# Kernel optimization log

Hardware: AMD Instinct MI355X
Metric: run time of the kernel (lower is better)

The kernel has to match this reference:

```python
import jax, jax.numpy as jnp
import numpy as np

N_NODES = 100000
N_EDGES = 1600000
IN_F, HID_F, N_CLS = 512, 128, 64


def spmm(row, col, val, x, n):
    # out[i] = sum_{e: row[e]==i} val[e] * x[col[e]]  (sparse adj @ x)
    msgs = val[:, None] * x[col]          # [E, F] gather + scale
    return jax.ops.segment_sum(msgs, row, num_segments=n)


def setup_inputs() -> dict:
    key = jax.random.key(0)
    k = jax.random.split(key, 8)
    x = jax.random.normal(k[0], (N_NODES, IN_F), dtype=jnp.float32)
    adj_row = jax.random.randint(k[1], (N_EDGES,), 0, N_NODES, dtype=jnp.int32)
    adj_col = jax.random.randint(k[2], (N_EDGES,), 0, N_NODES, dtype=jnp.int32)
    adj_val = jax.random.uniform(k[3], (N_EDGES,), dtype=jnp.float32)
    s1 = 1.0 / np.sqrt(IN_F)
    s2 = 1.0 / np.sqrt(HID_F)
    w1 = jax.random.uniform(k[4], (IN_F, HID_F), jnp.float32, -s1, s1)
    b1 = jax.random.uniform(k[5], (HID_F,), jnp.float32, -s1, s1)
    w2 = jax.random.uniform(k[6], (HID_F, N_CLS), jnp.float32, -s2, s2)
    b2 = jax.random.uniform(k[7], (N_CLS,), jnp.float32, -s2, s2)
    return {"x": x, "adj_row": adj_row, "adj_col": adj_col, "adj_val": adj_val,
            "w1": w1, "b1": b1, "w2": w2, "b2": b2}


def reference(x, adj_row, adj_col, adj_val, w1, b1, w2, b2):
    n = x.shape[0]
    # conv1: dense projection then sparse aggregation
    h = spmm(adj_row, adj_col, adj_val, x @ w1 + b1, n)
    h = jax.nn.relu(h)  # dropout is identity in eval mode
    # conv2
    out = spmm(adj_row, adj_col, adj_val, h @ w2 + b2, n)
    return out
```

## Files before the change

kernel.cpp:

```cpp
#include <hip/hip_runtime.h>
#include <hip/hip_bf16.h>


constexpr int N_NODES = 100000;
constexpr int IN_F    = 512;
constexpr int HID_F   = 128;
constexpr int N_CLS   = 64;
constexpr int N_EDGES = 1600000;

constexpr int SCAN_BLOCK    = 256;
constexpr int N_SCAN_BLOCKS = (N_NODES + SCAN_BLOCK - 1) / SCAN_BLOCK;
constexpr int N_WAVES_G     = N_NODES / 32;

typedef __attribute__((ext_vector_type(8))) short short8;
typedef __attribute__((ext_vector_type(4))) float f32x4;

static __device__ __forceinline__ unsigned short f2bf(float x) {
    unsigned int u = __float_as_uint(x);
    unsigned int r = (u + 0x7FFFu + ((u >> 16) & 1u)) >> 16;
    return (unsigned short)r;
}
static __device__ __forceinline__ float bf2f(unsigned short u) {
    return __uint_as_float(((unsigned int)u) << 16);
}

__global__ void w1t_kernel(const float* __restrict__ w1, unsigned short* __restrict__ w1t)
{
    int idx = blockIdx.x * 256 + threadIdx.x;
    int n = idx >> 9, k = idx & 511;
    w1t[idx] = f2bf(w1[k * HID_F + n]);
}

__global__ void w2t_kernel(const float* __restrict__ w2, unsigned short* __restrict__ w2t)
{
    int idx = blockIdx.x * 256 + threadIdx.x;
    int n = idx >> 7, k = idx & 127;
    w2t[idx] = f2bf(w2[k * N_CLS + n]);
}

__global__ void zero_int_kernel(int* __restrict__ p, int n)
{
    int i = blockIdx.x * blockDim.x + threadIdx.x;
    if (i < n) p[i] = 0;
}

__global__ void hist_kernel(const int* __restrict__ row, int* __restrict__ counts)
{
    int e = blockIdx.x * blockDim.x + threadIdx.x;
    if (e < N_EDGES) atomicAdd(&counts[row[e]], 1);
}

__global__ __launch_bounds__(SCAN_BLOCK) void scanA_kernel(
    const int* __restrict__ counts, int* __restrict__ local_ex,
    int* __restrict__ blockSums)
{
    __shared__ int s[SCAN_BLOCK];
    const int t = threadIdx.x;
    const int i = blockIdx.x * SCAN_BLOCK + t;
    int v = (i < N_NODES) ? counts[i] : 0;
    s[t] = v;
    __syncthreads();
    for (int off = 1; off < SCAN_BLOCK; off <<= 1) {
        int u = (t >= off) ? s[t - off] : 0;
        __syncthreads();
        s[t] += u;
        __syncthreads();
    }
    if (i < N_NODES) local_ex[i] = s[t] - v;
    if (t == SCAN_BLOCK - 1) blockSums[blockIdx.x] = s[t];
}

__global__ __launch_bounds__(512) void scanB_kernel(int* __restrict__ blockSums)
{
    __shared__ int s[512];
    const int t = threadIdx.x;
    int v = (t < N_SCAN_BLOCKS) ? blockSums[t] : 0;
    s[t] = v;
    __syncthreads();
    for (int off = 1; off < 512; off <<= 1) {
        int u = (t >= off) ? s[t - off] : 0;
        __syncthreads();
        s[t] += u;
        __syncthreads();
    }
    if (t < N_SCAN_BLOCKS) blockSums[t] = s[t] - v;
}

__global__ __launch_bounds__(SCAN_BLOCK) void scanC_kernel(
    const int* __restrict__ local_ex, const int* __restrict__ blockSums,
    int* __restrict__ row_ptr, int* __restrict__ cursor)
{
    const int i = blockIdx.x * SCAN_BLOCK + threadIdx.x;
    if (i < N_NODES) {
        int v = local_ex[i] + blockSums[blockIdx.x];
        row_ptr[i] = v;
        cursor[i]  = v;
    }
    if (i == 0) row_ptr[N_NODES] = N_EDGES;
}

__global__ void scatter_kernel(
    const int* __restrict__ row, const int* __restrict__ col,
    const float* __restrict__ val, int* __restrict__ cursor,
    int2* __restrict__ es)
{
    int e = blockIdx.x * blockDim.x + threadIdx.x;
    if (e < N_EDGES) {
        int pos = atomicAdd(&cursor[row[e]], 1);
        es[pos] = make_int2(col[e], __float_as_int(val[e]));
    }
}

__global__ __launch_bounds__(256) void gemm1_mfma_kernel(
    const float* __restrict__ x, const unsigned short* __restrict__ w1t,
    const float* __restrict__ b1, unsigned short* __restrict__ h0b)
{
    const int lane = threadIdx.x & 63;
    const int wid  = blockIdx.x * 4 + (threadIdx.x >> 6);
    if (wid >= N_WAVES_G) return;
    const int row0 = wid * 32;
    const int m = lane & 15;
    const int q = lane >> 4;

    f32x4 acc[2][8];
#pragma unroll
    for (int mi = 0; mi < 2; ++mi)
#pragma unroll
        for (int ni = 0; ni < 8; ++ni)
            acc[mi][ni] = (f32x4){0.f, 0.f, 0.f, 0.f};

    union U8 { short8 v; __hip_bfloat162 h[4]; };

    const float* a0p = x + (size_t)(row0 + m)      * IN_F + q * 8;
    const float* a1p = x + (size_t)(row0 + 16 + m) * IN_F + q * 8;
    const unsigned short* bp = w1t + (size_t)m * IN_F + q * 8;

    float4 c0l = ((const float4*)a0p)[0];
    float4 c0h = ((const float4*)a0p)[1];
    float4 c1l = ((const float4*)a1p)[0];
    float4 c1h = ((const float4*)a1p)[1];

    for (int kk = 0; kk < IN_F; kk += 32) {
        short8 bf[8];
#pragma unroll
        for (int ni = 0; ni < 8; ++ni)
            bf[ni] = *(const short8*)(bp + (size_t)ni * 16 * IN_F + kk);

        float4 n0l, n0h, n1l, n1h;
        if (kk + 32 < IN_F) {
            n0l = ((const float4*)(a0p + kk + 32))[0];
            n0h = ((const float4*)(a0p + kk + 32))[1];
            n1l = ((const float4*)(a1p + kk + 32))[0];
            n1h = ((const float4*)(a1p + kk + 32))[1];
        }

        U8 u0, u1;
        u0.h[0] = __float22bfloat162_rn(make_float2(c0l.x, c0l.y));
        u0.h[1] = __float22bfloat162_rn(make_float2(c0l.z, c0l.w));
        u0.h[2] = __float22bfloat162_rn(make_float2(c0h.x, c0h.y));
        u0.h[3] = __float22bfloat162_rn(make_float2(c0h.z, c0h.w));
        u1.h[0] = __float22bfloat162_rn(make_float2(c1l.x, c1l.y));
        u1.h[1] = __float22bfloat162_rn(make_float2(c1l.z, c1l.w));
        u1.h[2] = __float22bfloat162_rn(make_float2(c1h.x, c1h.y));
        u1.h[3] = __float22bfloat162_rn(make_float2(c1h.z, c1h.w));
        short8 a0 = u0.v, a1 = u1.v;

#pragma unroll
        for (int ni = 0; ni < 8; ++ni) {
            acc[0][ni] = __builtin_amdgcn_mfma_f32_16x16x32_bf16(a0, bf[ni], acc[0][ni], 0, 0, 0);
            acc[1][ni] = __builtin_amdgcn_mfma_f32_16x16x32_bf16(a1, bf[ni], acc[1][ni], 0, 0, 0);
        }

        c0l = n0l; c0h = n0h; c1l = n1l; c1h = n1h;
    }

    float bias[8];
#pragma unroll
    for (int ni = 0; ni < 8; ++ni) bias[ni] = b1[ni * 16 + m];

#pragma unroll
    for (int mi = 0; mi < 2; ++mi)
#pragma unroll
        for (int r = 0; r < 4; ++r) {
            int row = row0 + mi * 16 + q * 4 + r;
            unsigned short* dst = h0b + (size_t)row * HID_F;
#pragma unroll
            for (int ni = 0; ni < 8; ++ni)
                dst[ni * 16 + m] = f2bf(acc[mi][ni][r] + bias[ni]);
        }
}

__global__ __launch_bounds__(256) void gemm2_mfma_kernel(
    const unsigned short* __restrict__ h1r, const unsigned short* __restrict__ w2t,
    const float* __restrict__ b2, float* __restrict__ h2)
{
    const int lane = threadIdx.x & 63;
    const int wid  = blockIdx.x * 4 + (threadIdx.x >> 6);
    if (wid >= N_WAVES_G) return;
    const int row0 = wid * 32;
    const int m = lane & 15;
    const int q = lane >> 4;

    f32x4 acc[2][4];
#pragma unroll
    for (int mi = 0; mi < 2; ++mi)
#pragma unroll
        for (int ni = 0; ni < 4; ++ni)
            acc[mi][ni] = (f32x4){0.f, 0.f, 0.f, 0.f};

    const unsigned short* a0p = h1r + (size_t)(row0 + m)      * HID_F + q * 8;
    const unsigned short* a1p = h1r + (size_t)(row0 + 16 + m) * HID_F + q * 8;
    const unsigned short* bp  = w2t + (size_t)m * HID_F + q * 8;

#pragma unroll
    for (int t = 0; t < 4; ++t) {
        short8 a0 = *(const short8*)(a0p + t * 32);
        short8 a1 = *(const short8*)(a1p + t * 32);
#pragma unroll
        for (int ni = 0; ni < 4; ++ni) {
            short8 b = *(const short8*)(bp + (size_t)ni * 16 * HID_F + t * 32);
            acc[0][ni] = __builtin_amdgcn_mfma_f32_16x16x32_bf16(a0, b, acc[0][ni], 0, 0, 0);
            acc[1][ni] = __builtin_amdgcn_mfma_f32_16x16x32_bf16(a1, b, acc[1][ni], 0, 0, 0);
        }
    }

    float bias[4];
#pragma unroll
    for (int ni = 0; ni < 4; ++ni) bias[ni] = b2[ni * 16 + m];

#pragma unroll
    for (int mi = 0; mi < 2; ++mi)
#pragma unroll
        for (int r = 0; r < 4; ++r) {
            int row = row0 + mi * 16 + q * 4 + r;
            float* dst = h2 + (size_t)row * N_CLS;
#pragma unroll
            for (int ni = 0; ni < 4; ++ni)
                dst[ni * 16 + m] = acc[mi][ni][r] + bias[ni];
        }
}

__global__ __launch_bounds__(256) void spmm_g128_kernel(
    const int* __restrict__ rp, const int2* __restrict__ es,
    const unsigned short* __restrict__ src, unsigned short* __restrict__ dst)
{
    const int r = blockIdx.x * 4 + threadIdx.y;
    if (r >= N_NODES) return;
    const int lane = threadIdx.x;
    const int j0 = rp[r], j1 = rp[r + 1];

    float ax = 0.f, ay = 0.f;
    int j = j0;
    for (; j + 7 < j1; j += 8) {
        int2 e[8];
        ushort2 u[8];
#pragma unroll
        for (int t = 0; t < 8; ++t) e[t] = es[j + t];
#pragma unroll
        for (int t = 0; t < 8; ++t)
            u[t] = ((const ushort2*)(src + (size_t)e[t].x * HID_F))[lane];
#pragma unroll
        for (int t = 0; t < 8; ++t) {
            float v = __int_as_float(e[t].y);
            ax += v * bf2f(u[t].x);
            ay += v * bf2f(u[t].y);
        }
    }
    if (j + 3 < j1) {
        int2 e[4];
        ushort2 u[4];
#pragma unroll
        for (int t = 0; t < 4; ++t) e[t] = es[j + t];
#pragma unroll
        for (int t = 0; t < 4; ++t)
            u[t] = ((const ushort2*)(src + (size_t)e[t].x * HID_F))[lane];
#pragma unroll
        for (int t = 0; t < 4; ++t) {
            float v = __int_as_float(e[t].y);
            ax += v * bf2f(u[t].x);
            ay += v * bf2f(u[t].y);
        }
        j += 4;
    }
    for (; j < j1; ++j) {
        int2 e = es[j];
        float v = __int_as_float(e.y);
        ushort2 u = ((const ushort2*)(src + (size_t)e.x * HID_F))[lane];
        ax += v * bf2f(u.x);
        ay += v * bf2f(u.y);
    }
    ushort2 o;
    o.x = f2bf(fmaxf(ax, 0.f));
    o.y = f2bf(fmaxf(ay, 0.f));
    ((ushort2*)(dst + (size_t)r * HID_F))[lane] = o;
}

__global__ __launch_bounds__(256) void spmm_g64_kernel(
    const int* __restrict__ rp, const int2* __restrict__ es,
    const float* __restrict__ src, float* __restrict__ dst)
{
    const int r = blockIdx.x * 4 + threadIdx.y;
    if (r >= N_NODES) return;
    const int lane = threadIdx.x;
    const int j0 = rp[r], j1 = rp[r + 1];

    float acc = 0.f;
    int j = j0;
    for (; j + 7 < j1; j += 8) {
        int2 e[8];
        float a[8];
#pragma unroll
        for (int t = 0; t < 8; ++t) e[t] = es[j + t];
#pragma unroll
        for (int t = 0; t < 8; ++t)
            a[t] = src[(size_t)e[t].x * N_CLS + lane];
#pragma unroll
        for (int t = 0; t < 8; ++t)
            acc += __int_as_float(e[t].y) * a[t];
    }
    if (j + 3 < j1) {
        int2 e[4];
        float a[4];
#pragma unroll
        for (int t = 0; t < 4; ++t) e[t] = es[j + t];
#pragma unroll
        for (int t = 0; t < 4; ++t)
            a[t] = src[(size_t)e[t].x * N_CLS + lane];
#pragma unroll
        for (int t = 0; t < 4; ++t)
            acc += __int_as_float(e[t].y) * a[t];
        j += 4;
    }
    for (; j < j1; ++j) {
        int2 e = es[j];
        acc += __int_as_float(e.y) * src[(size_t)e.x * N_CLS + lane];
    }
    dst[(size_t)r * N_CLS + lane] = acc;
}

extern "C" void kernel_launch(void* const* d_in, const int* in_sizes, int n_in,
                              void* d_out, int out_size, void* d_ws, size_t ws_size,
                              hipStream_t stream)
{
    const float* x       = (const float*)d_in[0];
    const int*   adj_row = (const int*)  d_in[1];
    const int*   adj_col = (const int*)  d_in[2];
    const float* adj_val = (const float*)d_in[3];
    const float* w1      = (const float*)d_in[4];
    const float* b1      = (const float*)d_in[5];
    const float* w2      = (const float*)d_in[6];
    const float* b2      = (const float*)d_in[7];
    float*       out     = (float*)d_out;

    char* ws = (char*)d_ws;
    unsigned short* h0b   = (unsigned short*)ws;
    unsigned short* h1r   = (unsigned short*)(ws + 25600000);
    float*          h2    = (float*)(ws + 51200000);
    int2*           es    = (int2*) (ws + 76800000);
    int*            rp    = (int*)  (ws + 89600000);
    int*            cur   = (int*)  (ws + 90000016);
    unsigned short* w1t   = (unsigned short*)(ws + 90400016);
    int*            lex   = (int*)  (ws + 90531088);
    int*            bsum  = (int*)  (ws + 90931088);
    unsigned short* w2t   = (unsigned short*)(ws + 90932656);

    w1t_kernel<<<IN_F * HID_F / 256, 256, 0, stream>>>(w1, w1t);
    w2t_kernel<<<HID_F * N_CLS / 256, 256, 0, stream>>>(w2, w2t);
    zero_int_kernel<<<(N_NODES + 255) / 256, 256, 0, stream>>>(cur, N_NODES);
    hist_kernel<<<(N_EDGES + 255) / 256, 256, 0, stream>>>(adj_row, cur);
    scanA_kernel<<<N_SCAN_BLOCKS, SCAN_BLOCK, 0, stream>>>(cur, lex, bsum);
    scanB_kernel<<<1, 512, 0, stream>>>(bsum);
    scanC_kernel<<<N_SCAN_BLOCKS, SCAN_BLOCK, 0, stream>>>(lex, bsum, rp, cur);
    scatter_kernel<<<(N_EDGES + 255) / 256, 256, 0, stream>>>(
        adj_row, adj_col, adj_val, cur, es);

    gemm1_mfma_kernel<<<(N_WAVES_G + 3) / 4, 256, 0, stream>>>(x, w1t, b1, h0b);
    spmm_g128_kernel<<<(N_NODES + 3) / 4, dim3(64, 4), 0, stream>>>(
        rp, es, h0b, h1r);

    gemm2_mfma_kernel<<<(N_WAVES_G + 3) / 4, 256, 0, stream>>>(h1r, w2t, b2, h2);
    spmm_g64_kernel<<<(N_NODES + 3) / 4, dim3(64, 4), 0, stream>>>(
        rp, es, h2, out);
}
```

Before: 688.3 us.

## Stage GEMM weight tiles in swizzled LDS shared across 8-wave blocks

Result: faster. 660.1 us (-4.1%).

```diff
diff --git a/kernel.cpp b/kernel.cpp
--- a/kernel.cpp
+++ b/kernel.cpp
@@ -10,7 +10,7 @@
 
 constexpr int SCAN_BLOCK    = 256;
 constexpr int N_SCAN_BLOCKS = (N_NODES + SCAN_BLOCK - 1) / SCAN_BLOCK;
-constexpr int N_WAVES_G     = N_NODES / 32;
+constexpr int NB_GEMM       = (N_NODES + 255) / 256;
 
 typedef __attribute__((ext_vector_type(8))) short short8;
 typedef __attribute__((ext_vector_type(4))) float f32x4;
@@ -111,16 +111,20 @@
     }
 }
 
-__global__ __launch_bounds__(256) void gemm1_mfma_kernel(
+__global__ __launch_bounds__(512, 4) void gemm1_mfma_kernel(
     const float* __restrict__ x, const unsigned short* __restrict__ w1t,
     const float* __restrict__ b1, unsigned short* __restrict__ h0b)
 {
-    const int lane = threadIdx.x & 63;
-    const int wid  = blockIdx.x * 4 + (threadIdx.x >> 6);
-    if (wid >= N_WAVES_G) return;
-    const int row0 = wid * 32;
+    __shared__ unsigned short Bs[128 * 256];
+    char* lb = (char*)Bs;
+
+    const int tid  = threadIdx.x;
+    const int lane = tid & 63;
+    const int w    = tid >> 6;
     const int m = lane & 15;
     const int q = lane >> 4;
+    const int row0 = blockIdx.x * 256 + w * 32;
+    const bool active = row0 < N_NODES;
 
     f32x4 acc[2][8];
 #pragma unroll
@@ -133,46 +137,67 @@
 
     const float* a0p = x + (size_t)(row0 + m)      * IN_F + q * 8;
     const float* a1p = x + (size_t)(row0 + 16 + m) * IN_F + q * 8;
-    const unsigned short* bp = w1t + (size_t)m * IN_F + q * 8;
-
-    float4 c0l = ((const float4*)a0p)[0];
-    float4 c0h = ((const float4*)a0p)[1];
-    float4 c1l = ((const float4*)a1p)[0];
-    float4 c1h = ((const float4*)a1p)[1];
-
-    for (int kk = 0; kk < IN_F; kk += 32) {
-        short8 bf[8];
-#pragma unroll
-        for (int ni = 0; ni < 8; ++ni)
-            bf[ni] = *(const short8*)(bp + (size_t)ni * 16 * IN_F + kk);
-
-        float4 n0l, n0h, n1l, n1h;
-        if (kk + 32 < IN_F) {
-            n0l = ((const float4*)(a0p + kk + 32))[0];
-            n0h = ((const float4*)(a0p + kk + 32))[1];
-            n1l = ((const float4*)(a1p + kk + 32))[0];
-            n1h = ((const float4*)(a1p + kk + 32))[1];
-        }
-
-        U8 u0, u1;
-        u0.h[0] = __float22bfloat162_rn(make_float2(c0l.x, c0l.y));
-        u0.h[1] = __float22bfloat162_rn(make_float2(c0l.z, c0l.w));
-        u0.h[2] = __float22bfloat162_rn(make_float2(c0h.x, c0h.y));
-        u0.h[3] = __float22bfloat162_rn(make_float2(c0h.z, c0h.w));
-        u1.h[0] = __float22bfloat162_rn(make_float2(c1l.x, c1l.y));
-        u1.h[1] = __float22bfloat162_rn(make_float2(c1l.z, c1l.w));
-        u1.h[2] = __float22bfloat162_rn(make_float2(c1h.x, c1h.y));
-        u1.h[3] = __float22bfloat162_rn(make_float2(c1h.z, c1h.w));
-        short8 a0 = u0.v, a1 = u1.v;
-
-#pragma unroll
-        for (int ni = 0; ni < 8; ++ni) {
-            acc[0][ni] = __builtin_amdgcn_mfma_f32_16x16x32_bf16(a0, bf[ni], acc[0][ni], 0, 0, 0);
-            acc[1][ni] = __builtin_amdgcn_mfma_f32_16x16x32_bf16(a1, bf[ni], acc[1][ni], 0, 0, 0);
-        }
-
-        c0l = n0l; c0h = n0h; c1l = n1l; c1h = n1h;
-    }
+    const int swz = (m & 7) << 4;
+
+    for (int p = 0; p < 2; ++p) {
+        {
+            const unsigned short* src = w1t + p * 256;
+#pragma unroll
+            for (int i = 0; i < 8; ++i) {
+                int chunk = tid + i * 512;
+                int n   = chunk >> 5;
+                int k16 = chunk & 31;
+                short8 v = *(const short8*)(src + (size_t)n * IN_F + k16 * 8);
+                *(short8*)(lb + ((n * 512 + k16 * 16) ^ ((n & 7) << 4))) = v;
+            }
+        }
+        __syncthreads();
+
+        if (active) {
+            const float* a0 = a0p + p * 256;
+            const float* a1 = a1p + p * 256;
+            float4 c0l = ((const float4*)a0)[0];
+            float4 c0h = ((const float4*)a0)[1];
+            float4 c1l = ((const float4*)a1)[0];
+            float4 c1h = ((const float4*)a1)[1];
+
+#pragma unroll
+            for (int t = 0; t < 8; ++t) {
+                float4 n0l, n0h, n1l, n1h;
+                if (t + 1 < 8) {
+                    n0l = ((const float4*)(a0 + (t + 1) * 32))[0];
+                    n0h = ((const float4*)(a0 + (t + 1) * 32))[1];
+                    n1l = ((const float4*)(a1 + (t + 1) * 32))[0];
+                    n1h = ((const float4*)(a1 + (t + 1) * 32))[1];
+                }
+
+                U8 u0, u1;
+                u0.h[0] = __float22bfloat162_rn(make_float2(c0l.x, c0l.y));
+                u0.h[1] = __float22bfloat162_rn(make_float2(c0l.z, c0l.w));
+                u0.h[2] = __float22bfloat162_rn(make_float2(c0h.x, c0h.y));
+                u0.h[3] = __float22bfloat162_rn(make_float2(c0h.z, c0h.w));
+                u1.h[0] = __float22bfloat162_rn(make_float2(c1l.x, c1l.y));
+                u1.h[1] = __float22bfloat162_rn(make_float2(c1l.z, c1l.w));
+                u1.h[2] = __float22bfloat162_rn(make_float2(c1h.x, c1h.y));
+                u1.h[3] = __float22bfloat162_rn(make_float2(c1h.z, c1h.w));
+                short8 av0 = u0.v, av1 = u1.v;
+
+                const int kb = t * 64 + q * 16;
+#pragma unroll
+                for (int ni = 0; ni < 8; ++ni) {
+                    int off = (((ni * 16 + m) * 512) + kb) ^ swz;
+                    short8 bfr = *(const short8*)(lb + off);
+                    acc[0][ni] = __builtin_amdgcn_mfma_f32_16x16x32_bf16(av0, bfr, acc[0][ni], 0, 0, 0);
+                    acc[1][ni] = __builtin_amdgcn_mfma_f32_16x16x32_bf16(av1, bfr, acc[1][ni], 0, 0, 0);
+                }
+
+                c0l = n0l; c0h = n0h; c1l = n1l; c1h = n1h;
+            }
+        }
+        __syncthreads();
+    }
+
+    if (!active) return;
 
     float bias[8];
 #pragma unroll
@@ -190,16 +215,41 @@
         }
 }
 
-__global__ __launch_bounds__(256) void gemm2_mfma_kernel(
+__global__ __launch_bounds__(512, 4) void gemm2_mfma_kernel(
     const unsigned short* __restrict__ h1r, const unsigned short* __restrict__ w2t,
     const float* __restrict__ b2, float* __restrict__ h2)
 {
-    const int lane = threadIdx.x & 63;
-    const int wid  = blockIdx.x * 4 + (threadIdx.x >> 6);
-    if (wid >= N_WAVES_G) return;
-    const int row0 = wid * 32;
+    __shared__ unsigned short Bs[64 * 128];
+    char* lb = (char*)Bs;
+
+    const int tid  = threadIdx.x;
+    const int lane = tid & 63;
+    const int w    = tid >> 6;
     const int m = lane & 15;
     const int q = lane >> 4;
+    const int row0 = blockIdx.x * 256 + w * 32;
+    const bool active = row0 < N_NODES;
+
+#pragma unroll
+    for (int i = 0; i < 2; ++i) {
+        int chunk = tid + i * 512;
+        int n   = chunk >> 4;
+        int k16 = chunk & 15;
+        short8 v = *(const short8*)(w2t + (size_t)n * HID_F + k16 * 8);
+        *(short8*)(lb + ((n * 256 + k16 * 16) ^ ((n & 7) << 4))) = v;
+    }
+    __syncthreads();
+    if (!active) return;
+
+    const unsigned short* a0p = h1r + (size_t)(row0 + m)      * HID_F + q * 8;
+    const unsigned short* a1p = h1r + (size_t)(row0 + 16 + m) * HID_F + q * 8;
+
+    short8 a0[4], a1[4];
+#pragma unroll
+    for (int t = 0; t < 4; ++t) {
+        a0[t] = *(const short8*)(a0p + t * 32);
+        a1[t] = *(const short8*)(a1p + t * 32);
+    }
 
     f32x4 acc[2][4];
 #pragma unroll
@@ -208,19 +258,16 @@
         for (int ni = 0; ni < 4; ++ni)
             acc[mi][ni] = (f32x4){0.f, 0.f, 0.f, 0.f};
 
-    const unsigned short* a0p = h1r + (size_t)(row0 + m)      * HID_F + q * 8;
-    const unsigned short* a1p = h1r + (size_t)(row0 + 16 + m) * HID_F + q * 8;
-    const unsigned short* bp  = w2t + (size_t)m * HID_F + q * 8;
-
+    const int swz = (m & 7) << 4;
 #pragma unroll
     for (int t = 0; t < 4; ++t) {
-        short8 a0 = *(const short8*)(a0p + t * 32);
-        short8 a1 = *(const short8*)(a1p + t * 32);
+        const int kb = t * 64 + q * 16;
 #pragma unroll
         for (int ni = 0; ni < 4; ++ni) {
-            short8 b = *(const short8*)(bp + (size_t)ni * 16 * HID_F + t * 32);
-            acc[0][ni] = __builtin_amdgcn_mfma_f32_16x16x32_bf16(a0, b, acc[0][ni], 0, 0, 0);
-            acc[1][ni] = __builtin_amdgcn_mfma_f32_16x16x32_bf16(a1, b, acc[1][ni], 0, 0, 0);
+            int off = (((ni * 16 + m) * 256) + kb) ^ swz;
+            short8 b = *(const short8*)(lb + off);
+            acc[0][ni] = __builtin_amdgcn_mfma_f32_16x16x32_bf16(a0[t], b, acc[0][ni], 0, 0, 0);
+            acc[1][ni] = __builtin_amdgcn_mfma_f32_16x16x32_bf16(a1[t], b, acc[1][ni], 0, 0, 0);
         }
     }
 
@@ -374,11 +421,11 @@
     scatter_kernel<<<(N_EDGES + 255) / 256, 256, 0, stream>>>(
         adj_row, adj_col, adj_val, cur, es);
 
-    gemm1_mfma_kernel<<<(N_WAVES_G + 3) / 4, 256, 0, stream>>>(x, w1t, b1, h0b);
+    gemm1_mfma_kernel<<<NB_GEMM, 512, 0, stream>>>(x, w1t, b1, h0b);
     spmm_g128_kernel<<<(N_NODES + 3) / 4, dim3(64, 4), 0, stream>>>(
         rp, es, h0b, h1r);
 
-    gemm2_mfma_kernel<<<(N_WAVES_G + 3) / 4, 256, 0, stream>>>(h1r, w2t, b2, h2);
+    gemm2_mfma_kernel<<<NB_GEMM, 512, 0, stream>>>(h1r, w2t, b2, h2);
     spmm_g64_kernel<<<(N_NODES + 3) / 4, dim3(64, 4), 0, stream>>>(
         rp, es, h2, out);
 }
```
